# Optimization experiments

Measured on AMD Instinct MI355X. Metric: run time of the kernel, lower is better.

Reference implementation:

```python
import jax, jax.numpy as jnp
import numpy as np

DIM = 1024
HEADS = 16
B, N = 2, 2048


def setup_inputs() -> dict:
    key = jax.random.key(0)
    ks = jax.random.split(key, 10)
    s = 1.0 / np.sqrt(DIM)
    return {
        "y2_for": jax.random.normal(ks[0], (B, N, DIM), jnp.float32),
        "y2_back": jax.random.normal(ks[1], (B, N, DIM), jnp.float32),
        "Wq": jax.random.normal(ks[2], (DIM, DIM), jnp.float32) * s,
        "bq": jnp.zeros((DIM,), jnp.float32),
        "Wk": jax.random.normal(ks[3], (DIM, DIM), jnp.float32) * s,
        "bk": jnp.zeros((DIM,), jnp.float32),
        "Wv": jax.random.normal(ks[4], (DIM, DIM), jnp.float32) * s,
        "bv": jnp.zeros((DIM,), jnp.float32),
        "Wo": jax.random.normal(ks[5], (DIM, DIM), jnp.float32) * s,
        "bo": jnp.zeros((DIM,), jnp.float32),
    }


def reference(y2_for, y2_back, Wq, bq, Wk, bk, Wv, bv, Wo, bo):
    h = HEADS
    d = DIM // h
    scale = d ** -0.5
    q = y2_for @ Wq + bq                    # [b, n, dim]
    k = y2_back @ Wk + bk
    v = (y2_back + y2_for) @ Wv + bv

    def split_heads(x):
        b, n, _ = x.shape
        return x.reshape(b, n, h, d).transpose(0, 2, 1, 3)  # [b, h, n, d]

    q, k, v = split_heads(q), split_heads(k), split_heads(v)
    attn = jax.nn.softmax(jnp.einsum('bhid,bhjd->bhij', q, k) * scale, axis=-1)
    out = jnp.einsum('bhij,bhjd->bhid', attn, v)
    out = out.transpose(0, 2, 1, 3).reshape(y2_for.shape)   # [b, n, dim]
    out = out + y2_for + y2_back
    return out @ Wo + bo
```

## Files before the change

kernel.cpp:

```cpp
#include <hip/hip_runtime.h>

#define DIM 1024
#define HEADS 16
#define BB 2
#define NN 2048
#define HD 64
#define M_ROWS (BB*NN)

typedef __bf16 bf16x8 __attribute__((ext_vector_type(8)));
typedef float f32x4 __attribute__((ext_vector_type(4)));
typedef short s16x4 __attribute__((ext_vector_type(4)));

__device__ inline unsigned short f2bf(float f) {
    unsigned int u = __builtin_bit_cast(unsigned int, f);
    u += 0x7fffu + ((u >> 16) & 1u);
    return (unsigned short)(u >> 16);
}
__device__ inline float bf2f(unsigned short u) {
    return __builtin_bit_cast(float, (unsigned int)u << 16);
}
__device__ inline bf16x8 as_bf16x8(uint4 v) {
    return __builtin_bit_cast(bf16x8, v);
}
__device__ __forceinline__ void gl_lds16(const unsigned short* g, unsigned short* l) {
    __builtin_amdgcn_global_load_lds(
        (const __attribute__((address_space(1))) unsigned int*)g,
        (__attribute__((address_space(3))) unsigned int*)l, 16, 0, 0);
}

__device__ __forceinline__ f32x4 mfma16x16x16bf16(s16x4 a, s16x4 b, f32x4 c) {
#if __has_builtin(__builtin_amdgcn_mfma_f32_16x16x16bf16_1k)
    return __builtin_amdgcn_mfma_f32_16x16x16bf16_1k(a, b, c, 0, 0, 0);
#else
    asm volatile("v_mfma_f32_16x16x16_bf16 %0, %1, %2, %0"
                 : "+v"(c) : "v"(a), "v"(b));
    return c;
#endif
}

__global__ __launch_bounds__(256) void prep_all(
    const float* __restrict__ y2f, const float* __restrict__ y2b,
    const float* __restrict__ Wq, const float* __restrict__ Wk,
    const float* __restrict__ Wv, const float* __restrict__ Wo,
    unsigned short* __restrict__ Af, unsigned short* __restrict__ Ab,
    unsigned short* __restrict__ As, unsigned short* __restrict__ Wt_all)
{
    __shared__ float tile[32][33];
    const int blk = blockIdx.x;
    if (blk < 4096) {
        const int m = blk >> 10, r = blk & 1023, bk = r & 31, bn = r >> 5;
        const float* W = (m == 0) ? Wq : (m == 1) ? Wk : (m == 2) ? Wv : Wo;
        const int tx = threadIdx.x & 31, ty = threadIdx.x >> 5;
        #pragma unroll
        for (int i = 0; i < 32; i += 8)
            tile[ty + i][tx] = W[(size_t)(bk*32 + ty + i)*DIM + bn*32 + tx];
        __syncthreads();
        unsigned short* dst = Wt_all + (size_t)m * DIM * DIM;
        #pragma unroll
        for (int i = 0; i < 32; i += 8)
            dst[(size_t)(bn*32 + ty + i)*DIM + bk*32 + tx] = f2bf(tile[tx][ty + i]);
    } else {
        const size_t idx = ((size_t)(blk - 4096)*256 + threadIdx.x) * 8;
        #pragma unroll
        for (int half = 0; half < 2; half++) {
            float4 f = *(const float4*)(y2f + idx + half*4);
            float4 b = *(const float4*)(y2b + idx + half*4);
            ushort4 of, ob, os;
            of.x = f2bf(f.x); of.y = f2bf(f.y); of.z = f2bf(f.z); of.w = f2bf(f.w);
            ob.x = f2bf(b.x); ob.y = f2bf(b.y); ob.z = f2bf(b.z); ob.w = f2bf(b.w);
            os.x = f2bf(f.x + b.x); os.y = f2bf(f.y + b.y);
            os.z = f2bf(f.z + b.z); os.w = f2bf(f.w + b.w);
            *(ushort4*)(Af + idx + half*4) = of;
            *(ushort4*)(Ab + idx + half*4) = ob;
            *(ushort4*)(As + idx + half*4) = os;
        }
    }
}

__global__ __launch_bounds__(256) void gemm_qkv(
    const unsigned short* __restrict__ Af, const unsigned short* __restrict__ Ab,
    const unsigned short* __restrict__ As,
    const unsigned short* __restrict__ Wt_all,
    const float* __restrict__ bq, const float* __restrict__ bk,
    const float* __restrict__ bv,
    unsigned short* __restrict__ Qh, unsigned short* __restrict__ Kh,
    unsigned short* __restrict__ Vt)
{
    const int bm = blockIdx.x;
    const int mode = blockIdx.y >> 3;
    const int bn = blockIdx.y & 7;
    __shared__ __align__(16) unsigned short smem[3*8192];
    const int t = threadIdx.x;
    const int w = t >> 6, lane = t & 63, ln = lane & 15, quad = lane >> 4;
    const int wm = w >> 1, wn = w & 1;
    const unsigned short* Wt = Wt_all + (size_t)mode * (DIM*DIM);
    const unsigned short* A0 = (mode == 0) ? Af : (mode == 1) ? Ab : As;

    const int srow = lane >> 2;
    const int scol = (lane & 3) * 8;

    const unsigned short* gA0 = A0 + (size_t)(bm*128 + w*32 + srow)*DIM + scol;
    const unsigned short* gA1 = gA0 + (size_t)16*DIM;
    const unsigned short* gB0 = Wt + (size_t)(bn*128 + w*32 + srow)*DIM + scol;
    const unsigned short* gB1 = gB0 + (size_t)16*DIM;

    const int aoff = (wm*64 + ln)*32 + quad*8;
    const int boff = 4096 + (wn*64 + ln)*32 + quad*8;

    f32x4 acc[4][4];
    #pragma unroll
    for (int mi = 0; mi < 4; mi++)
        #pragma unroll
        for (int ni = 0; ni < 4; ni++)
            acc[mi][ni] = (f32x4){0.f, 0.f, 0.f, 0.f};

#define STAGE_Q(BUF) do { \
        unsigned short* s_ = smem + (BUF)*8192; \
        gl_lds16(gA0, &s_[(w*32)*32]); \
        gl_lds16(gA1, &s_[(w*32 + 16)*32]); \
        gl_lds16(gB0, &s_[4096 + (w*32)*32]); \
        gl_lds16(gB1, &s_[4096 + (w*32 + 16)*32]); \
        gA0 += 32; gA1 += 32; gB0 += 32; gB1 += 32; } while (0)

#define COMP_Q(BUF) do { \
        const unsigned short* s_ = smem + (BUF)*8192; \
        bf16x8 af[4], bfr[4]; \
        _Pragma("unroll") \
        for (int mi = 0; mi < 4; mi++) \
            af[mi] = as_bf16x8(*(const uint4*)(s_ + aoff + mi*512)); \
        _Pragma("unroll") \
        for (int ni = 0; ni < 4; ni++) \
            bfr[ni] = as_bf16x8(*(const uint4*)(s_ + boff + ni*512)); \
        _Pragma("unroll") \
        for (int mi = 0; mi < 4; mi++) \
            _Pragma("unroll") \
            for (int ni = 0; ni < 4; ni++) \
                acc[mi][ni] = __builtin_amdgcn_mfma_f32_16x16x32_bf16(af[mi], bfr[ni], acc[mi][ni], 0, 0, 0); \
    } while (0)

#define QITER(B) do { \
        asm volatile("s_waitcnt vmcnt(4)" ::: "memory"); \
        __builtin_amdgcn_s_barrier(); \
        __builtin_amdgcn_sched_barrier(0); \
        STAGE_Q(((B) + 2) % 3); \
        COMP_Q(B); \
        __builtin_amdgcn_sched_barrier(0); \
    } while (0)

    STAGE_Q(0);
    STAGE_Q(1);
    for (int base = 0; base < 30; base += 3) {
        QITER(0); QITER(1); QITER(2);
    }
    asm volatile("s_waitcnt vmcnt(4)" ::: "memory");
    __builtin_amdgcn_s_barrier();
    __builtin_amdgcn_sched_barrier(0);
    COMP_Q(0);
    __builtin_amdgcn_sched_barrier(0);
    asm volatile("s_waitcnt vmcnt(0)" ::: "memory");
    __builtin_amdgcn_s_barrier();
    __builtin_amdgcn_sched_barrier(0);
    COMP_Q(1);
#undef QITER
#undef COMP_Q
#undef STAGE_Q

    const float* bias = (mode == 0) ? bq : (mode == 1) ? bk : bv;
    unsigned short* dst = (mode == 0) ? Qh : (mode == 1) ? Kh : Vt;
    if (mode < 2) {
        const float sc = (mode == 0) ? 0.125f * 1.4426950408889634f : 1.0f;
        #pragma unroll
        for (int mi = 0; mi < 4; mi++) {
            #pragma unroll
            for (int r = 0; r < 4; r++) {
                int grow = bm*128 + wm*64 + mi*16 + quad*4 + r;
                int b_ = grow >> 11, n = grow & (NN - 1);
                #pragma unroll
                for (int ni = 0; ni < 4; ni++) {
                    int gcol = bn*128 + wn*64 + ni*16 + ln;
                    int hh = gcol >> 6, dd = gcol & 63;
                    float val = (acc[mi][ni][r] + bias[gcol]) * sc;
                    dst[(((size_t)(b_*HEADS + hh))*NN + n)*HD + dd] = f2bf(val);
                }
            }
        }
    } else {
        __syncthreads();
        #pragma unroll
        for (int ni = 0; ni < 4; ni++) {
            int row_s = wn*64 + ni*16 + ln;
            float bsv = bias[bn*128 + row_s];
            int sxor = (row_s & 7) << 1;
            #pragma unroll
            for (int mi = 0; mi < 4; mi++) {
                int u = wm*16 + mi*4 + quad;
                ushort4 pk;
                pk.x = f2bf(acc[mi][ni][0] + bsv);
                pk.y = f2bf(acc[mi][ni][1] + bsv);
                pk.z = f2bf(acc[mi][ni][2] + bsv);
                pk.w = f2bf(acc[mi][ni][3] + bsv);
                *(ushort4*)(&smem[row_s*128 + ((u ^ sxor) << 2)]) = pk;
            }
        }
        __syncthreads();
        const int b_ = bm >> 4;
        #pragma unroll
        for (int i = 0; i < 8; i++) {
            int idx = i*256 + t;
            int dd = idx >> 4, jc = idx & 15;
            int u = (jc*2) ^ ((dd & 7) << 1);
            int hh = bn*2 + (dd >> 6), d_ = dd & 63;
            *(uint4*)(dst + (((size_t)(b_*HEADS + hh))*HD + d_)*NN
                          + (size_t)(bm & 15)*128 + jc*8)
                = *(const uint4*)(&smem[dd*128 + (u << 2)]);
        }
    }
}

__global__ __launch_bounds__(256) void gemm_out(
    const unsigned short* __restrict__ attp,
    const unsigned short* __restrict__ Wt_all,
    const float* __restrict__ bo, float* __restrict__ out)
{
    const int bm = blockIdx.x, bn = blockIdx.y;
    __shared__ __align__(16) unsigned short smem[3*6144];
    const int t = threadIdx.x;
    const int w = t >> 6, lane = t & 63, ln = lane & 15, quad = lane >> 4;
    const int wm = w >> 1, wn = w & 1;
    const unsigned short* Wt = Wt_all + (size_t)3 * (DIM*DIM);

    const int srow = lane >> 2;
    const int scol = (lane & 3) * 8;

    const unsigned short* gA = attp + (size_t)(bm*64 + w*16 + srow)*DIM + scol;
    const unsigned short* gB0 = Wt + (size_t)(bn*128 + w*32 + srow)*DIM + scol;
    const unsigned short* gB1 = gB0 + (size_t)16*DIM;

    const int aoff = (wm*32 + ln)*32 + quad*8;
    const int boff = 2048 + (wn*64 + ln)*32 + quad*8;

    f32x4 acc[2][4];
    #pragma unroll
    for (int mi = 0; mi < 2; mi++)
        #pragma unroll
        for (int ni = 0; ni < 4; ni++)
            acc[mi][ni] = (f32x4){0.f, 0.f, 0.f, 0.f};

#define STAGE_T(BUF) do { \
        unsigned short* s_ = smem + (BUF)*6144; \
        gl_lds16(gA, &s_[(w*16)*32]); \
        gl_lds16(gB0, &s_[2048 + (w*32)*32]); \
        gl_lds16(gB1, &s_[2048 + (w*32 + 16)*32]); \
        gA += 32; gB0 += 32; gB1 += 32; } while (0)

#define COMP_T(BUF) do { \
        const unsigned short* s_ = smem + (BUF)*6144; \
        bf16x8 af[2], bfr[4]; \
        _Pragma("unroll") \
        for (int mi = 0; mi < 2; mi++) \
            af[mi] = as_bf16x8(*(const uint4*)(s_ + aoff + mi*512)); \
        _Pragma("unroll") \
        for (int ni = 0; ni < 4; ni++) \
            bfr[ni] = as_bf16x8(*(const uint4*)(s_ + boff + ni*512)); \
        _Pragma("unroll") \
        for (int mi = 0; mi < 2; mi++) \
            _Pragma("unroll") \
            for (int ni = 0; ni < 4; ni++) \
                acc[mi][ni] = __builtin_amdgcn_mfma_f32_16x16x32_bf16(af[mi], bfr[ni], acc[mi][ni], 0, 0, 0); \
    } while (0)

#define TITER(B) do { \
        asm volatile("s_waitcnt vmcnt(3)" ::: "memory"); \
        __builtin_amdgcn_s_barrier(); \
        __builtin_amdgcn_sched_barrier(0); \
        STAGE_T(((B) + 2) % 3); \
        COMP_T(B); \
        __builtin_amdgcn_sched_barrier(0); \
    } while (0)

    STAGE_T(0);
    STAGE_T(1);
    for (int base = 0; base < 30; base += 3) {
        TITER(0); TITER(1); TITER(2);
    }
    asm volatile("s_waitcnt vmcnt(3)" ::: "memory");
    __builtin_amdgcn_s_barrier();
    __builtin_amdgcn_sched_barrier(0);
    COMP_T(0);
    __builtin_amdgcn_sched_barrier(0);
    asm volatile("s_waitcnt vmcnt(0)" ::: "memory");
    __builtin_amdgcn_s_barrier();
    __builtin_amdgcn_sched_barrier(0);
    COMP_T(1);
#undef TITER
#undef COMP_T
#undef STAGE_T

    #pragma unroll
    for (int mi = 0; mi < 2; mi++) {
        #pragma unroll
        for (int r = 0; r < 4; r++) {
            int grow = bm*64 + wm*32 + mi*16 + quad*4 + r;
            #pragma unroll
            for (int ni = 0; ni < 4; ni++) {
                int gcol = bn*128 + wn*64 + ni*16 + ln;
                out[(size_t)grow*DIM + gcol] = acc[mi][ni][r] + bo[gcol];
            }
        }
    }
}

__global__ __launch_bounds__(256) void attn_kernel(
    const unsigned short* __restrict__ Qh, const unsigned short* __restrict__ Kh,
    const unsigned short* __restrict__ Vt, const unsigned short* __restrict__ As,
    unsigned short* __restrict__ attp)
{
    const int bh = blockIdx.x;
    const int qt = blockIdx.y;
    const int b = bh >> 4, h = bh & 15;
    const int t = threadIdx.x;
    const int w = t >> 6, lane = t & 63, ln = lane & 15, quad = lane >> 4;
    const int sw = ln & 7;
    const float EBIAS = 17.312340490667562f;

    __shared__ __align__(16) unsigned short sK[2][64*64];
    __shared__ __align__(16) unsigned short sVt[2][64*64];

    const unsigned short* Qb  = Qh + (size_t)bh * NN * HD + (size_t)qt * 64 * HD;
    const unsigned short* Kb  = Kh + (size_t)bh * NN * HD;
    const unsigned short* Vtb = Vt + (size_t)bh * HD * NN;

    const int rl = lane >> 3, cb = lane & 7;

    bf16x8 aq[2];
    #pragma unroll
    for (int k = 0; k < 2; k++)
        aq[k] = as_bf16x8(*(const uint4*)(Qb + (size_t)(w*16 + ln)*HD + (k*4 + quad)*8));

    const int r0 = w*16 + rl, r1 = w*16 + 8 + rl;
    const unsigned short* gK0 = Kb + (size_t)r0*HD + (cb ^ (r0 & 7))*8;
    const unsigned short* gK1 = Kb + (size_t)r1*HD + (cb ^ (r1 & 7))*8;
    const unsigned short* gV0 = Vtb + (size_t)r0*NN + (cb ^ (r0 & 7))*8;
    const unsigned short* gV1 = Vtb + (size_t)r1*NN + (cb ^ (r1 & 7))*8;

#define STAGE_KV(BUF) do { \
        gl_lds16(gK0, &sK[BUF][(w*16)*64]); \
        gl_lds16(gK1, &sK[BUF][(w*16 + 8)*64]); \
        gl_lds16(gV0, &sVt[BUF][(w*16)*64]); \
        gl_lds16(gV1, &sVt[BUF][(w*16 + 8)*64]); \
        gK0 += 64*HD; gK1 += 64*HD; gV0 += 64; gV1 += 64; } while (0)

    const int kc0 = ((quad ^ (sw & 3)) + 4*((sw >> 2) & 1)) * 8;
    const unsigned short* bK0a = &sK[0][ln*64 + kc0];
    const unsigned short* bK0b = &sK[0][ln*64 + (kc0 ^ 32)];
    const unsigned short* bK1a = &sK[1][ln*64 + kc0];
    const unsigned short* bK1b = &sK[1][ln*64 + (kc0 ^ 32)];
    const int vb = ln*64 + ((quad >> 1) ^ (sw & 1))*8 + (quad & 1)*4;
    const int sv = (sw >> 1) & 3;
    const unsigned short* bV0_0 = &sVt[0][vb + (0 ^ sv)*16];
    const unsigned short* bV0_1 = &sVt[0][vb + (1 ^ sv)*16];
    const unsigned short* bV0_2 = &sVt[0][vb + (2 ^ sv)*16];
    const unsigned short* bV0_3 = &sVt[0][vb + (3 ^ sv)*16];
    const unsigned short* bV1_0 = &sVt[1][vb + (0 ^ sv)*16];
    const unsigned short* bV1_1 = &sVt[1][vb + (1 ^ sv)*16];
    const unsigned short* bV1_2 = &sVt[1][vb + (2 ^ sv)*16];
    const unsigned short* bV1_3 = &sVt[1][vb + (3 ^ sv)*16];

    const s16x4 ones = { (short)0x3F80, (short)0x3F80, (short)0x3F80, (short)0x3F80 };
    f32x4 accO[4], accL;
    accL = (f32x4){0.f, 0.f, 0.f, 0.f};
    #pragma unroll
    for (int di = 0; di < 4; di++) accO[di] = (f32x4){0.f, 0.f, 0.f, 0.f};

#define ATT_JT(PK0_, PK1_, PV0_, PV1_, PV2_, PV3_) do { \
        f32x4 accS[4]; \
        _Pragma("unroll") \
        for (int ni = 0; ni < 4; ni++) \
            accS[ni] = (f32x4){-EBIAS, -EBIAS, -EBIAS, -EBIAS}; \
        __builtin_amdgcn_s_setprio(1); \
        _Pragma("unroll") \
        for (int ni = 0; ni < 4; ni++) { \
            bf16x8 b0_ = as_bf16x8(*(const uint4*)(PK0_ + ni*1024)); \
            accS[ni] = __builtin_amdgcn_mfma_f32_16x16x32_bf16(b0_, aq[0], accS[ni], 0, 0, 0); \
            bf16x8 b1_ = as_bf16x8(*(const uint4*)(PK1_ + ni*1024)); \
            accS[ni] = __builtin_amdgcn_mfma_f32_16x16x32_bf16(b1_, aq[1], accS[ni], 0, 0, 0); \
        } \
        __builtin_amdgcn_s_setprio(0); \
        s16x4 pf[4]; \
        _Pragma("unroll") \
        for (int ni = 0; ni < 4; ni++) { \
            unsigned int e0 = __builtin_bit_cast(unsigned int, __builtin_amdgcn_exp2f(accS[ni][0])); \
            unsigned int e1 = __builtin_bit_cast(unsigned int, __builtin_amdgcn_exp2f(accS[ni][1])); \
            unsigned int e2 = __builtin_bit_cast(unsigned int, __builtin_amdgcn_exp2f(accS[ni][2])); \
            unsigned int e3 = __builtin_bit_cast(unsigned int, __builtin_amdgcn_exp2f(accS[ni][3])); \
            unsigned int lo = __builtin_amdgcn_perm(e1, e0, 0x07060302u); \
            unsigned int hi = __builtin_amdgcn_perm(e3, e2, 0x07060302u); \
            pf[ni] = __builtin_bit_cast(s16x4, uint2{lo, hi}); \
            accL = mfma16x16x16bf16(pf[ni], ones, accL); \
        } \
        __builtin_amdgcn_s_setprio(1); \
        _Pragma("unroll") \
        for (int ni = 0; ni < 4; ni++) { \
            const unsigned short* pv_ = (ni == 0) ? PV0_ : (ni == 1) ? PV1_ \
                                      : (ni == 2) ? PV2_ : PV3_; \
            _Pragma("unroll") \
            for (int di = 0; di < 4; di++) \
                accO[di] = mfma16x16x16bf16(pf[ni], \
                    __builtin_bit_cast(s16x4, *(const uint2*)(pv_ + di*1024)), accO[di]); \
        } \
        __builtin_amdgcn_s_setprio(0); \
    } while (0)

#define ATT_SYNC() do { \
        __builtin_amdgcn_sched_barrier(0); \
        asm volatile("s_waitcnt vmcnt(0)" ::: "memory"); \
        __builtin_amdgcn_s_barrier(); \
        __builtin_amdgcn_sched_barrier(0); \
    } while (0)

    STAGE_KV(0);
    ATT_SYNC();
    for (int jt2 = 0; jt2 < 15; jt2++) {
        STAGE_KV(1);
        ATT_JT(bK0a, bK0b, bV0_0, bV0_1, bV0_2, bV0_3);
        ATT_SYNC();
        STAGE_KV(0);
        ATT_JT(bK1a, bK1b, bV1_0, bV1_1, bV1_2, bV1_3);
        ATT_SYNC();
    }
    STAGE_KV(1);
    ATT_JT(bK0a, bK0b, bV0_0, bV0_1, bV0_2, bV0_3);
    ATT_SYNC();
    ATT_JT(bK1a, bK1b, bV1_0, bV1_1, bV1_2, bV1_3);
#undef ATT_SYNC
#undef ATT_JT
#undef STAGE_KV

    #pragma unroll
    for (int r = 0; r < 4; r++) {
        float inv = 1.f / accL[r];
        int n = qt*64 + w*16 + quad*4 + r;
        #pragma unroll
        for (int di = 0; di < 4; di++) {
            int c = h*64 + di*16 + ln;
            size_t gi = ((size_t)b*NN + n)*DIM + c;
            float o = accO[di][r]*inv + bf2f(As[gi]);
            attp[gi] = f2bf(o);
        }
    }
}

extern "C" void kernel_launch(void* const* d_in, const int* in_sizes, int n_in,
                              void* d_out, int out_size, void* d_ws, size_t ws_size,
                              hipStream_t stream) {
    const float* y2f = (const float*)d_in[0];
    const float* y2b = (const float*)d_in[1];
    const float* Wq  = (const float*)d_in[2];
    const float* bq  = (const float*)d_in[3];
    const float* Wk  = (const float*)d_in[4];
    const float* bk  = (const float*)d_in[5];
    const float* Wv  = (const float*)d_in[6];
    const float* bv  = (const float*)d_in[7];
    const float* Wo  = (const float*)d_in[8];
    const float* bo  = (const float*)d_in[9];
    float* out = (float*)d_out;

    const size_t NACT = (size_t)M_ROWS * DIM;
    unsigned short* ws   = (unsigned short*)d_ws;
    unsigned short* Af   = ws;
    unsigned short* Ab   = ws + NACT;
    unsigned short* As   = ws + 2*NACT;
    unsigned short* Qh   = ws + 3*NACT;
    unsigned short* Kh   = ws + 4*NACT;
    unsigned short* Vt   = ws + 5*NACT;
    unsigned short* Wt   = ws + 6*NACT;
    unsigned short* attp = Ab;

    prep_all<<<dim3(6144), 256, 0, stream>>>(y2f, y2b, Wq, Wk, Wv, Wo,
                                             Af, Ab, As, Wt);
    gemm_qkv<<<dim3(32, 24), 256, 0, stream>>>(
        Af, Ab, As, Wt, bq, bk, bv, Qh, Kh, Vt);
    attn_kernel<<<dim3(32, 32), 256, 0, stream>>>(Qh, Kh, Vt, As, attp);
    gemm_out<<<dim3(64, 8), 256, 0, stream>>>(attp, Wt, bo, out);
}
```

Before: 218.8 us.

## Process two 64-row query tiles per attention block to reuse staged K/V

Each attention block now handles 128 query rows (two sub-tiles per wave) instead of 64, so every K/V tile staged into shared memory feeds twice as many MFMAs. The grid is halved to 32x16 blocks. This cuts global K/V traffic and per-tile sync overhead per query, but it doubles accumulator and register pressure and halves the block count (512 blocks), which may lower occupancy. The loop is also rewritten with inline swizzle address computation in place of precomputed pointers.

After: 218.7 us. Within noise of the previous version (-0.0%).

```diff
diff --git a/kernel.cpp b/kernel.cpp
--- a/kernel.cpp
+++ b/kernel.cpp
@@ -326,126 +326,124 @@
     __shared__ __align__(16) unsigned short sK[2][64*64];
     __shared__ __align__(16) unsigned short sVt[2][64*64];
 
-    const unsigned short* Qb  = Qh + (size_t)bh * NN * HD + (size_t)qt * 64 * HD;
+    const unsigned short* Qb  = Qh + (size_t)bh * NN * HD + (size_t)qt * 128 * HD;
     const unsigned short* Kb  = Kh + (size_t)bh * NN * HD;
     const unsigned short* Vtb = Vt + (size_t)bh * HD * NN;
 
     const int rl = lane >> 3, cb = lane & 7;
 
-    bf16x8 aq[2];
-    #pragma unroll
-    for (int k = 0; k < 2; k++)
-        aq[k] = as_bf16x8(*(const uint4*)(Qb + (size_t)(w*16 + ln)*HD + (k*4 + quad)*8));
-
-    const int r0 = w*16 + rl, r1 = w*16 + 8 + rl;
-    const unsigned short* gK0 = Kb + (size_t)r0*HD + (cb ^ (r0 & 7))*8;
-    const unsigned short* gK1 = Kb + (size_t)r1*HD + (cb ^ (r1 & 7))*8;
-    const unsigned short* gV0 = Vtb + (size_t)r0*NN + (cb ^ (r0 & 7))*8;
-    const unsigned short* gV1 = Vtb + (size_t)r1*NN + (cb ^ (r1 & 7))*8;
-
-#define STAGE_KV(BUF) do { \
-        gl_lds16(gK0, &sK[BUF][(w*16)*64]); \
-        gl_lds16(gK1, &sK[BUF][(w*16 + 8)*64]); \
-        gl_lds16(gV0, &sVt[BUF][(w*16)*64]); \
-        gl_lds16(gV1, &sVt[BUF][(w*16 + 8)*64]); \
-        gK0 += 64*HD; gK1 += 64*HD; gV0 += 64; gV1 += 64; } while (0)
-
-    const int kc0 = ((quad ^ (sw & 3)) + 4*((sw >> 2) & 1)) * 8;
-    const unsigned short* bK0a = &sK[0][ln*64 + kc0];
-    const unsigned short* bK0b = &sK[0][ln*64 + (kc0 ^ 32)];
-    const unsigned short* bK1a = &sK[1][ln*64 + kc0];
-    const unsigned short* bK1b = &sK[1][ln*64 + (kc0 ^ 32)];
-    const int vb = ln*64 + ((quad >> 1) ^ (sw & 1))*8 + (quad & 1)*4;
-    const int sv = (sw >> 1) & 3;
-    const unsigned short* bV0_0 = &sVt[0][vb + (0 ^ sv)*16];
-    const unsigned short* bV0_1 = &sVt[0][vb + (1 ^ sv)*16];
-    const unsigned short* bV0_2 = &sVt[0][vb + (2 ^ sv)*16];
-    const unsigned short* bV0_3 = &sVt[0][vb + (3 ^ sv)*16];
-    const unsigned short* bV1_0 = &sVt[1][vb + (0 ^ sv)*16];
-    const unsigned short* bV1_1 = &sVt[1][vb + (1 ^ sv)*16];
-    const unsigned short* bV1_2 = &sVt[1][vb + (2 ^ sv)*16];
-    const unsigned short* bV1_3 = &sVt[1][vb + (3 ^ sv)*16];
+    bf16x8 aq[2][2];
+    #pragma unroll
+    for (int m = 0; m < 2; m++)
+        #pragma unroll
+        for (int k = 0; k < 2; k++)
+            aq[m][k] = as_bf16x8(*(const uint4*)(
+                Qb + (size_t)(m*64 + w*16 + ln)*HD + (k*4 + quad)*8));
+
+#define STAGE_KV(JT, BBUF) do { \
+        _Pragma("unroll") \
+        for (int j = 0; j < 2; j++) { \
+            int row = w*16 + j*8 + rl; \
+            gl_lds16(Kb + (size_t)((JT)*64 + row)*HD + ((cb ^ (row & 7))*8), \
+                     &sK[BBUF][(w*16 + j*8)*64]); \
+            gl_lds16(Vtb + (size_t)row*NN + (JT)*64 + ((cb ^ (row & 7))*8), \
+                     &sVt[BBUF][(w*16 + j*8)*64]); \
+        } } while (0)
 
     const s16x4 ones = { (short)0x3F80, (short)0x3F80, (short)0x3F80, (short)0x3F80 };
-    f32x4 accO[4], accL;
-    accL = (f32x4){0.f, 0.f, 0.f, 0.f};
-    #pragma unroll
-    for (int di = 0; di < 4; di++) accO[di] = (f32x4){0.f, 0.f, 0.f, 0.f};
-
-#define ATT_JT(PK0_, PK1_, PV0_, PV1_, PV2_, PV3_) do { \
-        f32x4 accS[4]; \
-        _Pragma("unroll") \
-        for (int ni = 0; ni < 4; ni++) \
-            accS[ni] = (f32x4){-EBIAS, -EBIAS, -EBIAS, -EBIAS}; \
-        __builtin_amdgcn_s_setprio(1); \
-        _Pragma("unroll") \
-        for (int ni = 0; ni < 4; ni++) { \
-            bf16x8 b0_ = as_bf16x8(*(const uint4*)(PK0_ + ni*1024)); \
-            accS[ni] = __builtin_amdgcn_mfma_f32_16x16x32_bf16(b0_, aq[0], accS[ni], 0, 0, 0); \
-            bf16x8 b1_ = as_bf16x8(*(const uint4*)(PK1_ + ni*1024)); \
-            accS[ni] = __builtin_amdgcn_mfma_f32_16x16x32_bf16(b1_, aq[1], accS[ni], 0, 0, 0); \
-        } \
-        __builtin_amdgcn_s_setprio(0); \
-        s16x4 pf[4]; \
-        _Pragma("unroll") \
-        for (int ni = 0; ni < 4; ni++) { \
-            unsigned int e0 = __builtin_bit_cast(unsigned int, __builtin_amdgcn_exp2f(accS[ni][0])); \
-            unsigned int e1 = __builtin_bit_cast(unsigned int, __builtin_amdgcn_exp2f(accS[ni][1])); \
-            unsigned int e2 = __builtin_bit_cast(unsigned int, __builtin_amdgcn_exp2f(accS[ni][2])); \
-            unsigned int e3 = __builtin_bit_cast(unsigned int, __builtin_amdgcn_exp2f(accS[ni][3])); \
-            unsigned int lo = __builtin_amdgcn_perm(e1, e0, 0x07060302u); \
-            unsigned int hi = __builtin_amdgcn_perm(e3, e2, 0x07060302u); \
-            pf[ni] = __builtin_bit_cast(s16x4, uint2{lo, hi}); \
-            accL = mfma16x16x16bf16(pf[ni], ones, accL); \
-        } \
-        __builtin_amdgcn_s_setprio(1); \
-        _Pragma("unroll") \
-        for (int ni = 0; ni < 4; ni++) { \
-            const unsigned short* pv_ = (ni == 0) ? PV0_ : (ni == 1) ? PV1_ \
-                                      : (ni == 2) ? PV2_ : PV3_; \
-            _Pragma("unroll") \
-            for (int di = 0; di < 4; di++) \
-                accO[di] = mfma16x16x16bf16(pf[ni], \
-                    __builtin_bit_cast(s16x4, *(const uint2*)(pv_ + di*1024)), accO[di]); \
-        } \
-        __builtin_amdgcn_s_setprio(0); \
-    } while (0)
-
-#define ATT_SYNC() do { \
-        __builtin_amdgcn_sched_barrier(0); \
-        asm volatile("s_waitcnt vmcnt(0)" ::: "memory"); \
-        __builtin_amdgcn_s_barrier(); \
-        __builtin_amdgcn_sched_barrier(0); \
-    } while (0)
-
-    STAGE_KV(0);
-    ATT_SYNC();
-    for (int jt2 = 0; jt2 < 15; jt2++) {
-        STAGE_KV(1);
-        ATT_JT(bK0a, bK0b, bV0_0, bV0_1, bV0_2, bV0_3);
-        ATT_SYNC();
-        STAGE_KV(0);
-        ATT_JT(bK1a, bK1b, bV1_0, bV1_1, bV1_2, bV1_3);
-        ATT_SYNC();
-    }
-    STAGE_KV(1);
-    ATT_JT(bK0a, bK0b, bV0_0, bV0_1, bV0_2, bV0_3);
-    ATT_SYNC();
-    ATT_JT(bK1a, bK1b, bV1_0, bV1_1, bV1_2, bV1_3);
-#undef ATT_SYNC
-#undef ATT_JT
+    f32x4 accO[2][4], accL[2];
+    #pragma unroll
+    for (int m = 0; m < 2; m++) {
+        accL[m] = (f32x4){0.f, 0.f, 0.f, 0.f};
+        #pragma unroll
+        for (int di = 0; di < 4; di++) accO[m][di] = (f32x4){0.f, 0.f, 0.f, 0.f};
+    }
+
+    STAGE_KV(0, 0);
+    asm volatile("s_waitcnt vmcnt(0)" ::: "memory");
+    __builtin_amdgcn_s_barrier();
+    __builtin_amdgcn_sched_barrier(0);
+
+    #pragma unroll 2
+    for (int jt = 0; jt < 32; jt++) {
+        const int cur = jt & 1;
+        if (jt < 31) STAGE_KV(jt + 1, cur ^ 1);
+
+        const unsigned short* sKc = sK[cur];
+        const unsigned short* sVc = sVt[cur];
+
+        f32x4 accS[2][4];
+        #pragma unroll
+        for (int m = 0; m < 2; m++)
+            #pragma unroll
+            for (int ni = 0; ni < 4; ni++)
+                accS[m][ni] = (f32x4){-EBIAS, -EBIAS, -EBIAS, -EBIAS};
+        __builtin_amdgcn_s_setprio(1);
+        #pragma unroll
+        for (int ni = 0; ni < 4; ni++) {
+            bf16x8 b0 = as_bf16x8(*(const uint4*)(
+                &sKc[(ni*16 + ln)*64 + (((0 + quad) ^ sw)*8)]));
+            accS[0][ni] = __builtin_amdgcn_mfma_f32_16x16x32_bf16(b0, aq[0][0], accS[0][ni], 0, 0, 0);
+            accS[1][ni] = __builtin_amdgcn_mfma_f32_16x16x32_bf16(b0, aq[1][0], accS[1][ni], 0, 0, 0);
+            bf16x8 b1 = as_bf16x8(*(const uint4*)(
+                &sKc[(ni*16 + ln)*64 + (((4 + quad) ^ sw)*8)]));
+            accS[0][ni] = __builtin_amdgcn_mfma_f32_16x16x32_bf16(b1, aq[0][1], accS[0][ni], 0, 0, 0);
+            accS[1][ni] = __builtin_amdgcn_mfma_f32_16x16x32_bf16(b1, aq[1][1], accS[1][ni], 0, 0, 0);
+        }
+        __builtin_amdgcn_s_setprio(0);
+
+        s16x4 pf[2][4];
+        #pragma unroll
+        for (int m = 0; m < 2; m++)
+            #pragma unroll
+            for (int ni = 0; ni < 4; ni++) {
+                unsigned int e0 = __builtin_bit_cast(unsigned int, __builtin_amdgcn_exp2f(accS[m][ni][0]));
+                unsigned int e1 = __builtin_bit_cast(unsigned int, __builtin_amdgcn_exp2f(accS[m][ni][1]));
+                unsigned int e2 = __builtin_bit_cast(unsigned int, __builtin_amdgcn_exp2f(accS[m][ni][2]));
+                unsigned int e3 = __builtin_bit_cast(unsigned int, __builtin_amdgcn_exp2f(accS[m][ni][3]));
+                unsigned int lo = __builtin_amdgcn_perm(e1, e0, 0x07060302u);
+                unsigned int hi = __builtin_amdgcn_perm(e3, e2, 0x07060302u);
+                pf[m][ni] = __builtin_bit_cast(s16x4, uint2{lo, hi});
+                accL[m] = mfma16x16x16bf16(pf[m][ni], ones, accL[m]);
+            }
+
+        __builtin_amdgcn_s_setprio(1);
+        #pragma unroll
+        for (int ni = 0; ni < 4; ni++) {
+            int blkv = 2*ni + (quad >> 1);
+            int off = (quad & 1) * 4;
+            #pragma unroll
+            for (int di = 0; di < 4; di++) {
+                s16x4 bv = __builtin_bit_cast(s16x4,
+                    *(const uint2*)(&sVc[(di*16 + ln)*64 + ((blkv ^ sw)*8) + off]));
+                accO[0][di] = mfma16x16x16bf16(pf[0][ni], bv, accO[0][di]);
+                accO[1][di] = mfma16x16x16bf16(pf[1][ni], bv, accO[1][di]);
+            }
+        }
+        __builtin_amdgcn_s_setprio(0);
+
+        __builtin_amdgcn_sched_barrier(0);
+        if (jt < 31) {
+            asm volatile("s_waitcnt vmcnt(0)" ::: "memory");
+            __builtin_amdgcn_s_barrier();
+            __builtin_amdgcn_sched_barrier(0);
+        }
+    }
 #undef STAGE_KV
 
     #pragma unroll
-    for (int r = 0; r < 4; r++) {
-        float inv = 1.f / accL[r];
-        int n = qt*64 + w*16 + quad*4 + r;
-        #pragma unroll
-        for (int di = 0; di < 4; di++) {
-            int c = h*64 + di*16 + ln;
-            size_t gi = ((size_t)b*NN + n)*DIM + c;
-            float o = accO[di][r]*inv + bf2f(As[gi]);
-            attp[gi] = f2bf(o);
+    for (int m = 0; m < 2; m++) {
+        #pragma unroll
+        for (int r = 0; r < 4; r++) {
+            float inv = 1.f / accL[m][r];
+            int n = qt*128 + m*64 + w*16 + quad*4 + r;
+            #pragma unroll
+            for (int di = 0; di < 4; di++) {
+                int c = h*64 + di*16 + ln;
+                size_t gi = ((size_t)b*NN + n)*DIM + c;
+                float o = accO[m][di][r]*inv + bf2f(As[gi]);
+                attp[gi] = f2bf(o);
+            }
         }
     }
 }
@@ -480,6 +478,6 @@
                                              Af, Ab, As, Wt);
     gemm_qkv<<<dim3(32, 24), 256, 0, stream>>>(
         Af, Ab, As, Wt, bq, bk, bv, Qh, Kh, Vt);
-    attn_kernel<<<dim3(32, 32), 256, 0, stream>>>(Qh, Kh, Vt, As, attp);
+    attn_kernel<<<dim3(32, 16), 256, 0, stream>>>(Qh, Kh, Vt, As, attp);
     gemm_out<<<dim3(64, 8), 256, 0, stream>>>(attp, Wt, bo, out);
 }
```

## Double query tile per block and software-pipeline QK with softmax-PV over 4-stage KV ring

Applied to the files above, without the earlier changes.

Each attention block now handles 128 query rows (two 64-row tiles), so every K/V tile loaded into shared memory is reused twice and the grid shrinks to 512 blocks. The K/V staging becomes a 4-buffer ring with partial vmcnt waits. The QK^T of the next tile is interleaved with the exp/PV of the previous one, so matrix and transcendental work overlap. The cost is more registers (two sets of score accumulators and doubled output accumulators), more LDS, fewer blocks to fill the GPU, and the setprio hints are gone.

After: 217.7 us. No clear change (-0.5%).

```diff
diff --git a/kernel.cpp b/kernel.cpp
--- a/kernel.cpp
+++ b/kernel.cpp
@@ -323,21 +323,24 @@
     const int sw = ln & 7;
     const float EBIAS = 17.312340490667562f;
 
-    __shared__ __align__(16) unsigned short sK[2][64*64];
-    __shared__ __align__(16) unsigned short sVt[2][64*64];
-
-    const unsigned short* Qb  = Qh + (size_t)bh * NN * HD + (size_t)qt * 64 * HD;
+    __shared__ __align__(16) unsigned short sK[4][64*64];
+    __shared__ __align__(16) unsigned short sVt[4][64*64];
+
+    const unsigned short* Qb  = Qh + (size_t)bh * NN * HD + (size_t)qt * 128 * HD;
     const unsigned short* Kb  = Kh + (size_t)bh * NN * HD;
     const unsigned short* Vtb = Vt + (size_t)bh * HD * NN;
 
     const int rl = lane >> 3, cb = lane & 7;
 
-    bf16x8 aq[2];
-    #pragma unroll
-    for (int k = 0; k < 2; k++)
-        aq[k] = as_bf16x8(*(const uint4*)(Qb + (size_t)(w*16 + ln)*HD + (k*4 + quad)*8));
-
-    const int r0 = w*16 + rl, r1 = w*16 + 8 + rl;
+    bf16x8 aq[2][2];
+    #pragma unroll
+    for (int m = 0; m < 2; m++)
+        #pragma unroll
+        for (int k = 0; k < 2; k++)
+            aq[m][k] = as_bf16x8(*(const uint4*)(
+                Qb + (size_t)(m*64 + w*16 + ln)*HD + (k*4 + quad)*8));
+
+    const int r0 = w*16 + rl, r1 = r0 + 8;
     const unsigned short* gK0 = Kb + (size_t)r0*HD + (cb ^ (r0 & 7))*8;
     const unsigned short* gK1 = Kb + (size_t)r1*HD + (cb ^ (r1 & 7))*8;
     const unsigned short* gV0 = Vtb + (size_t)r0*NN + (cb ^ (r0 & 7))*8;
@@ -350,102 +353,101 @@
         gl_lds16(gV1, &sVt[BUF][(w*16 + 8)*64]); \
         gK0 += 64*HD; gK1 += 64*HD; gV0 += 64; gV1 += 64; } while (0)
 
-    const int kc0 = ((quad ^ (sw & 3)) + 4*((sw >> 2) & 1)) * 8;
-    const unsigned short* bK0a = &sK[0][ln*64 + kc0];
-    const unsigned short* bK0b = &sK[0][ln*64 + (kc0 ^ 32)];
-    const unsigned short* bK1a = &sK[1][ln*64 + kc0];
-    const unsigned short* bK1b = &sK[1][ln*64 + (kc0 ^ 32)];
-    const int vb = ln*64 + ((quad >> 1) ^ (sw & 1))*8 + (quad & 1)*4;
-    const int sv = (sw >> 1) & 3;
-    const unsigned short* bV0_0 = &sVt[0][vb + (0 ^ sv)*16];
-    const unsigned short* bV0_1 = &sVt[0][vb + (1 ^ sv)*16];
-    const unsigned short* bV0_2 = &sVt[0][vb + (2 ^ sv)*16];
-    const unsigned short* bV0_3 = &sVt[0][vb + (3 ^ sv)*16];
-    const unsigned short* bV1_0 = &sVt[1][vb + (0 ^ sv)*16];
-    const unsigned short* bV1_1 = &sVt[1][vb + (1 ^ sv)*16];
-    const unsigned short* bV1_2 = &sVt[1][vb + (2 ^ sv)*16];
-    const unsigned short* bV1_3 = &sVt[1][vb + (3 ^ sv)*16];
-
     const s16x4 ones = { (short)0x3F80, (short)0x3F80, (short)0x3F80, (short)0x3F80 };
-    f32x4 accO[4], accL;
-    accL = (f32x4){0.f, 0.f, 0.f, 0.f};
-    #pragma unroll
-    for (int di = 0; di < 4; di++) accO[di] = (f32x4){0.f, 0.f, 0.f, 0.f};
-
-#define ATT_JT(PK0_, PK1_, PV0_, PV1_, PV2_, PV3_) do { \
-        f32x4 accS[4]; \
-        _Pragma("unroll") \
-        for (int ni = 0; ni < 4; ni++) \
-            accS[ni] = (f32x4){-EBIAS, -EBIAS, -EBIAS, -EBIAS}; \
-        __builtin_amdgcn_s_setprio(1); \
+    f32x4 accO[2][4], accL[2];
+    #pragma unroll
+    for (int m = 0; m < 2; m++) {
+        accL[m] = (f32x4){0.f, 0.f, 0.f, 0.f};
+        #pragma unroll
+        for (int di = 0; di < 4; di++) accO[m][di] = (f32x4){0.f, 0.f, 0.f, 0.f};
+    }
+    f32x4 accSA[2][4], accSB[2][4];
+
+#define QK_TILE(BUF, ACCS) do { \
+        _Pragma("unroll") \
+        for (int m = 0; m < 2; m++) \
+            _Pragma("unroll") \
+            for (int ni = 0; ni < 4; ni++) \
+                ACCS[m][ni] = (f32x4){-EBIAS, -EBIAS, -EBIAS, -EBIAS}; \
         _Pragma("unroll") \
         for (int ni = 0; ni < 4; ni++) { \
-            bf16x8 b0_ = as_bf16x8(*(const uint4*)(PK0_ + ni*1024)); \
-            accS[ni] = __builtin_amdgcn_mfma_f32_16x16x32_bf16(b0_, aq[0], accS[ni], 0, 0, 0); \
-            bf16x8 b1_ = as_bf16x8(*(const uint4*)(PK1_ + ni*1024)); \
-            accS[ni] = __builtin_amdgcn_mfma_f32_16x16x32_bf16(b1_, aq[1], accS[ni], 0, 0, 0); \
-        } \
-        __builtin_amdgcn_s_setprio(0); \
-        s16x4 pf[4]; \
+            bf16x8 b0_ = as_bf16x8(*(const uint4*)( \
+                &sK[BUF][(ni*16 + ln)*64 + ((quad ^ sw)*8)])); \
+            ACCS[0][ni] = __builtin_amdgcn_mfma_f32_16x16x32_bf16(b0_, aq[0][0], ACCS[0][ni], 0, 0, 0); \
+            ACCS[1][ni] = __builtin_amdgcn_mfma_f32_16x16x32_bf16(b0_, aq[1][0], ACCS[1][ni], 0, 0, 0); \
+            bf16x8 b1_ = as_bf16x8(*(const uint4*)( \
+                &sK[BUF][(ni*16 + ln)*64 + (((4 + quad) ^ sw)*8)])); \
+            ACCS[0][ni] = __builtin_amdgcn_mfma_f32_16x16x32_bf16(b1_, aq[0][1], ACCS[0][ni], 0, 0, 0); \
+            ACCS[1][ni] = __builtin_amdgcn_mfma_f32_16x16x32_bf16(b1_, aq[1][1], ACCS[1][ni], 0, 0, 0); \
+        } } while (0)
+
+#define SOFTPV_TILE(BUF, ACCS) do { \
+        s16x4 pf[2][4]; \
+        _Pragma("unroll") \
+        for (int m = 0; m < 2; m++) \
+            _Pragma("unroll") \
+            for (int ni = 0; ni < 4; ni++) { \
+                unsigned int e0 = __builtin_bit_cast(unsigned int, __builtin_amdgcn_exp2f(ACCS[m][ni][0])); \
+                unsigned int e1 = __builtin_bit_cast(unsigned int, __builtin_amdgcn_exp2f(ACCS[m][ni][1])); \
+                unsigned int e2 = __builtin_bit_cast(unsigned int, __builtin_amdgcn_exp2f(ACCS[m][ni][2])); \
+                unsigned int e3 = __builtin_bit_cast(unsigned int, __builtin_amdgcn_exp2f(ACCS[m][ni][3])); \
+                unsigned int lo = __builtin_amdgcn_perm(e1, e0, 0x07060302u); \
+                unsigned int hi = __builtin_amdgcn_perm(e3, e2, 0x07060302u); \
+                pf[m][ni] = __builtin_bit_cast(s16x4, uint2{lo, hi}); \
+                accL[m] = mfma16x16x16bf16(pf[m][ni], ones, accL[m]); \
+            } \
         _Pragma("unroll") \
         for (int ni = 0; ni < 4; ni++) { \
-            unsigned int e0 = __builtin_bit_cast(unsigned int, __builtin_amdgcn_exp2f(accS[ni][0])); \
-            unsigned int e1 = __builtin_bit_cast(unsigned int, __builtin_amdgcn_exp2f(accS[ni][1])); \
-            unsigned int e2 = __builtin_bit_cast(unsigned int, __builtin_amdgcn_exp2f(accS[ni][2])); \
-            unsigned int e3 = __builtin_bit_cast(unsigned int, __builtin_amdgcn_exp2f(accS[ni][3])); \
-            unsigned int lo = __builtin_amdgcn_perm(e1, e0, 0x07060302u); \
-            unsigned int hi = __builtin_amdgcn_perm(e3, e2, 0x07060302u); \
-            pf[ni] = __builtin_bit_cast(s16x4, uint2{lo, hi}); \
-            accL = mfma16x16x16bf16(pf[ni], ones, accL); \
-        } \
-        __builtin_amdgcn_s_setprio(1); \
-        _Pragma("unroll") \
-        for (int ni = 0; ni < 4; ni++) { \
-            const unsigned short* pv_ = (ni == 0) ? PV0_ : (ni == 1) ? PV1_ \
-                                      : (ni == 2) ? PV2_ : PV3_; \
+            int blkv = 2*ni + (quad >> 1); \
+            int off = (quad & 1) * 4; \
             _Pragma("unroll") \
-            for (int di = 0; di < 4; di++) \
-                accO[di] = mfma16x16x16bf16(pf[ni], \
-                    __builtin_bit_cast(s16x4, *(const uint2*)(pv_ + di*1024)), accO[di]); \
-        } \
-        __builtin_amdgcn_s_setprio(0); \
-    } while (0)
-
-#define ATT_SYNC() do { \
-        __builtin_amdgcn_sched_barrier(0); \
-        asm volatile("s_waitcnt vmcnt(0)" ::: "memory"); \
+            for (int di = 0; di < 4; di++) { \
+                s16x4 bv = __builtin_bit_cast(s16x4, \
+                    *(const uint2*)(&sVt[BUF][(di*16 + ln)*64 + ((blkv ^ sw)*8) + off])); \
+                accO[0][di] = mfma16x16x16bf16(pf[0][ni], bv, accO[0][di]); \
+                accO[1][di] = mfma16x16x16bf16(pf[1][ni], bv, accO[1][di]); \
+            } \
+        } } while (0)
+
+#define KV_SYNC(VM) do { \
+        asm volatile("s_waitcnt vmcnt(" #VM ")" ::: "memory"); \
         __builtin_amdgcn_s_barrier(); \
-        __builtin_amdgcn_sched_barrier(0); \
-    } while (0)
+        __builtin_amdgcn_sched_barrier(0); } while (0)
 
     STAGE_KV(0);
-    ATT_SYNC();
-    for (int jt2 = 0; jt2 < 15; jt2++) {
-        STAGE_KV(1);
-        ATT_JT(bK0a, bK0b, bV0_0, bV0_1, bV0_2, bV0_3);
-        ATT_SYNC();
-        STAGE_KV(0);
-        ATT_JT(bK1a, bK1b, bV1_0, bV1_1, bV1_2, bV1_3);
-        ATT_SYNC();
-    }
     STAGE_KV(1);
-    ATT_JT(bK0a, bK0b, bV0_0, bV0_1, bV0_2, bV0_3);
-    ATT_SYNC();
-    ATT_JT(bK1a, bK1b, bV1_0, bV1_1, bV1_2, bV1_3);
-#undef ATT_SYNC
-#undef ATT_JT
+    KV_SYNC(4);
+    STAGE_KV(2);
+    QK_TILE(0, accSA);
+    #pragma unroll 1
+    for (int g = 0; g < 7; ++g) {
+        KV_SYNC(4); STAGE_KV(3); QK_TILE(1, accSB); SOFTPV_TILE(0, accSA);
+        KV_SYNC(4); STAGE_KV(0); QK_TILE(2, accSA); SOFTPV_TILE(1, accSB);
+        KV_SYNC(4); STAGE_KV(1); QK_TILE(3, accSB); SOFTPV_TILE(2, accSA);
+        KV_SYNC(4); STAGE_KV(2); QK_TILE(0, accSA); SOFTPV_TILE(3, accSB);
+    }
+    KV_SYNC(4); STAGE_KV(3); QK_TILE(1, accSB); SOFTPV_TILE(0, accSA);
+    KV_SYNC(4);              QK_TILE(2, accSA); SOFTPV_TILE(1, accSB);
+    KV_SYNC(0);              QK_TILE(3, accSB); SOFTPV_TILE(2, accSA);
+    SOFTPV_TILE(3, accSB);
+#undef KV_SYNC
+#undef SOFTPV_TILE
+#undef QK_TILE
 #undef STAGE_KV
 
     #pragma unroll
-    for (int r = 0; r < 4; r++) {
-        float inv = 1.f / accL[r];
-        int n = qt*64 + w*16 + quad*4 + r;
-        #pragma unroll
-        for (int di = 0; di < 4; di++) {
-            int c = h*64 + di*16 + ln;
-            size_t gi = ((size_t)b*NN + n)*DIM + c;
-            float o = accO[di][r]*inv + bf2f(As[gi]);
-            attp[gi] = f2bf(o);
+    for (int m = 0; m < 2; m++) {
+        #pragma unroll
+        for (int r = 0; r < 4; r++) {
+            float inv = 1.f / accL[m][r];
+            int n = qt*128 + m*64 + w*16 + quad*4 + r;
+            #pragma unroll
+            for (int di = 0; di < 4; di++) {
+                int c = h*64 + di*16 + ln;
+                size_t gi = ((size_t)b*NN + n)*DIM + c;
+                float o = accO[m][di][r]*inv + bf2f(As[gi]);
+                attp[gi] = f2bf(o);
+            }
         }
     }
 }
@@ -480,6 +482,6 @@
                                              Af, Ab, As, Wt);
     gemm_qkv<<<dim3(32, 24), 256, 0, stream>>>(
         Af, Ab, As, Wt, bq, bk, bv, Qh, Kh, Vt);
-    attn_kernel<<<dim3(32, 32), 256, 0, stream>>>(Qh, Kh, Vt, As, attp);
+    attn_kernel<<<dim3(32, 16), 256, 0, stream>>>(Qh, Kh, Vt, As, attp);
     gemm_out<<<dim3(64, 8), 256, 0, stream>>>(attp, Wt, bo, out);
 }
```
